# Kernel optimization log

Measured on AMD Instinct MI355X. Metric: run time of the kernel, lower is better.

## Reference

```python
import jax, jax.numpy as jnp
import numpy as np
import math

B, N, H, TDIM, K, R = 32, 4096, 256, 128, 2, 2


def setup_inputs() -> dict:
    key = jax.random.key(0)
    ks = jax.random.split(key, 12)
    s = 1.0 / math.sqrt(H)
    gain = 1.414
    return {
        "x": jax.random.normal(ks[0], (B, N), jnp.float32),
        "t": jax.random.uniform(ks[1], (B,), jnp.float32),
        # scaled so repeated L@x stays O(1) over Chebyshev hops
        "laplacian": jax.random.normal(ks[2], (N, N), jnp.float32) / math.sqrt(N),
        "w_g1": jax.random.normal(ks[3], (1, H, K + 1), jnp.float32) * gain / math.sqrt(1 + H),
        "w_g2": jax.random.normal(ks[4], (H, 1, K + 1), jnp.float32) * gain / math.sqrt(1 + H),
        "w_t1": jax.random.normal(ks[5], (TDIM, H), jnp.float32) / math.sqrt(TDIM),
        "b_t1": jnp.zeros((H,), jnp.float32),
        "w_t2": jax.random.normal(ks[6], (H, H), jnp.float32) * s,
        "b_t2": jnp.zeros((H,), jnp.float32),
        "w_map": jax.random.normal(ks[7], (N, H), jnp.float32) / math.sqrt(N),
        "b_map": jnp.zeros((H,), jnp.float32),
        "res_w": jax.random.normal(ks[8], (R, 3, H, H), jnp.float32) * s,
        "res_b": jnp.zeros((R, 3, H), jnp.float32),
        "w_o1": jax.random.normal(ks[9], (H, H), jnp.float32) * s,
        "b_o1": jnp.zeros((H,), jnp.float32),
        "w_o2": jax.random.normal(ks[10], (H, N), jnp.float32) * s,
        "b_o2": jnp.zeros((N,), jnp.float32),
    }


def timestep_embedding(t, dim, max_period=10000):
    half = dim // 2  # dim is even here
    freqs = jnp.exp(-math.log(max_period) * jnp.arange(half, dtype=t.dtype) / half)
    args = t[:, None] * freqs[None, :]  # [B, half]
    return jnp.concatenate([jnp.cos(args), jnp.sin(args)], axis=-1)  # [B, dim]


def gcn_layer(L, x, w, conv_order):
    xs = [x]
    h = x
    for _ in range(conv_order):
        h = jnp.einsum('mn,bnc->bmc', L, h)  # sparse-style Laplacian propagation (dense here)
        xs.append(h)
    X = jnp.stack(xs, axis=-1)  # [B, N, C, K+1]
    return jnp.einsum('bnik,iok->bno', X, w)


def reference(x, t, laplacian, w_g1, w_g2, w_t1, b_t1, w_t2, b_t2,
              w_map, b_map, res_w, res_b, w_o1, b_o1, w_o2, b_o2):
    silu = jax.nn.silu
    # time embedding path: sinusoidal -> Linear -> SiLU -> Linear
    temb = timestep_embedding(t, TDIM)
    t_out = silu(temb @ w_t1 + b_t1) @ w_t2 + b_t2  # [B, H]
    # GCNBlock: two Chebyshev GCN layers (GCNLayer.forward applies no activation)
    g = gcn_layer(laplacian, x[:, :, None], w_g1, K)  # [B, N, H]
    g = gcn_layer(laplacian, g, w_g2, K)[..., 0]      # [B, N]
    # ResNet_FC on the node signal
    h = g @ w_map + b_map  # [B, H]
    inv_sqrt2 = 1.0 / math.sqrt(2.0)
    for r in range(R):
        z = h
        for i in range(3):
            z = silu(z @ res_w[r, i] + res_b[r, i])
        h = (h + z) * inv_sqrt2
    # output head with time conditioning
    out = silu((h + t_out) @ w_o1 + b_o1) @ w_o2 + b_o2  # [B, N]
    return out
```

## Files before the change

### kernel.cpp

```cpp
#include <hip/hip_runtime.h>
#include <hip/hip_bf16.h>

typedef __bf16 bf16x8 __attribute__((ext_vector_type(8)));
typedef __bf16 bf16x4 __attribute__((ext_vector_type(4)));
typedef float  f32x4  __attribute__((ext_vector_type(4)));


static constexpr size_t WS_A     = 0;
static constexpr size_t WS_TOUT  = 1024;
static constexpr size_t WS_Z1    = 65536;
static constexpr size_t WS_ZSTR  = 524288;
static constexpr size_t WS_H0    = WS_Z1 + 4 * WS_ZSTR;
static constexpr size_t WS_G2F   = WS_H0 + 32768;
static constexpr size_t WS_UB    = WS_G2F + 524288;
static constexpr size_t WS_WMAPT = 2752512;
static constexpr size_t WS_WO2T  = WS_WMAPT + 2097152;
static constexpr size_t WS_LBF   = 8388608;

__device__ __forceinline__ f32x4 mfma16(bf16x8 a, bf16x8 b, f32x4 c) {
    return __builtin_amdgcn_mfma_f32_16x16x32_bf16(a, b, c, 0, 0, 0);
}

__device__ __forceinline__ bf16x8 pack8(f32x4 lo, f32x4 hi) {
    bf16x8 r;
    r[0] = (__bf16)lo[0]; r[1] = (__bf16)lo[1]; r[2] = (__bf16)lo[2]; r[3] = (__bf16)lo[3];
    r[4] = (__bf16)hi[0]; r[5] = (__bf16)hi[1]; r[6] = (__bf16)hi[2]; r[7] = (__bf16)hi[3];
    return r;
}

__device__ __forceinline__ bf16x8 cvt8(const float* p) {
    return pack8(*(const f32x4*)p, *(const f32x4*)(p + 4));
}

__device__ __forceinline__ float silu_f(float x) { return x / (1.0f + __expf(-x)); }

template <int NST>
__device__ __forceinline__ float dotW(const float* __restrict__ W,
                                      const float* __restrict__ zs, int col) {
    float wb[2][16];
#pragma unroll
    for (int u = 0; u < 16; ++u) wb[0][u] = W[u * 256 + col];
    float a0 = 0, a1 = 0, a2 = 0, a3 = 0;
#pragma unroll
    for (int g = 0; g < NST; ++g) {
        const int cur = g & 1, nxt = cur ^ 1;
        if (g < NST - 1) {
#pragma unroll
            for (int u = 0; u < 16; ++u) wb[nxt][u] = W[((g + 1) * 16 + u) * 256 + col];
        }
        const float* z = zs + g * 16;
#pragma unroll
        for (int u = 0; u < 16; u += 4) {
            a0 += z[u]     * wb[cur][u];
            a1 += z[u + 1] * wb[cur][u + 1];
            a2 += z[u + 2] * wb[cur][u + 2];
            a3 += z[u + 3] * wb[cur][u + 3];
        }
    }
    return (a0 + a1) + (a2 + a3);
}

__device__ __forceinline__ void transpose_tile(const float* __restrict__ src, int sstride,
                                               __bf16* __restrict__ dst, int dstride,
                                               int r0, int c0, float* sh, int tid) {
    const int r = tid >> 3, cg = (tid & 7) * 4;
    f32x4 v = *(const f32x4*)(src + (size_t)(r0 + r) * sstride + c0 + cg);
    sh[r * 33 + cg + 0] = v[0];
    sh[r * 33 + cg + 1] = v[1];
    sh[r * 33 + cg + 2] = v[2];
    sh[r * 33 + cg + 3] = v[3];
    __syncthreads();
    bf16x4 o;
    o[0] = (__bf16)sh[(cg + 0) * 33 + r];
    o[1] = (__bf16)sh[(cg + 1) * 33 + r];
    o[2] = (__bf16)sh[(cg + 2) * 33 + r];
    o[3] = (__bf16)sh[(cg + 3) * 33 + r];
    *(bf16x4*)(dst + (size_t)(c0 + r) * dstride + r0 + cg) = o;
}

static constexpr int PG_LCVT  = 8192;
static constexpr int PG_COEF  = PG_LCVT;
static constexpr int PG_TMLP  = PG_COEF + 1;
static constexpr int PG_WMAP  = PG_TMLP + 32;
static constexpr int PG_WO2   = PG_WMAP + 1024;
static constexpr int PG_TOTAL = PG_WO2 + 1024;

__global__ __launch_bounds__(256) void prep_kernel(
    const float* __restrict__ t, const float* __restrict__ L,
    const float* __restrict__ w_g1, const float* __restrict__ w_g2,
    const float* __restrict__ w_t1, const float* __restrict__ b_t1,
    const float* __restrict__ w_t2, const float* __restrict__ b_t2,
    const float* __restrict__ w_map, const float* __restrict__ w_o2,
    char* __restrict__ ws)
{
    __shared__ float sh[1056];
    const int bi = blockIdx.x, tid = threadIdx.x;
    if (bi < PG_LCVT) {
        const size_t base = (size_t)bi * 2048 + (size_t)tid * 8;
        *(bf16x8*)((__bf16*)(ws + WS_LBF) + base) = cvt8(L + base);
    } else if (bi == PG_COEF) {
        if (tid < 9) {
            const int k1 = tid / 3, k2 = tid % 3;
            float s = 0.f;
            for (int h = 0; h < 256; ++h) s += w_g1[h * 3 + k1] * w_g2[h * 3 + k2];
            sh[tid] = s;
        }
        __syncthreads();
        if (tid == 0) {
            float* a = (float*)(ws + WS_A);
            a[0] = sh[0];
            a[1] = sh[1] + sh[3];
            a[2] = sh[2] + sh[4] + sh[6];
            a[3] = sh[5] + sh[7];
            a[4] = sh[8];
        }
    } else if (bi < PG_WMAP) {
        const int b = bi - PG_TMLP;
        float* t_out = (float*)(ws + WS_TOUT);
        if (tid < 64) {
            float fr = __expf(-9.210340371976184f * (float)tid * (1.0f / 64.0f));
            float ang = t[b] * fr;
            sh[tid]      = __cosf(ang);
            sh[64 + tid] = __sinf(ang);
        }
        __syncthreads();
        float h1 = silu_f(b_t1[tid] + dotW<8>(w_t1, sh, tid));
        sh[128 + tid] = h1;
        __syncthreads();
        t_out[b * 256 + tid] = b_t2[tid] + dotW<16>(w_t2, sh + 128, tid);
    } else if (bi < PG_WO2) {
        const int ti = bi - PG_WMAP;
        transpose_tile(w_map, 256, (__bf16*)(ws + WS_WMAPT), 4096,
                       (ti >> 3) * 32, (ti & 7) * 32, sh, tid);
    } else {
        const int ti = bi - PG_WO2;
        transpose_tile(w_o2, 4096, (__bf16*)(ws + WS_WO2T), 256,
                       (ti & 7) * 32, (ti >> 3) * 32, sh, tid);
    }
}

__device__ __forceinline__ void hop_core(
    const __bf16* __restrict__ Lb, const float* __restrict__ zin,
    float (*red)[16][33], int bi, int tid, float v[2])
{
    const int wave = tid >> 6, lane = tid & 63;
    const int l15 = lane & 15, q = lane >> 4;
    const int m0 = bi * 16;
    const int kbase = wave * 1024 + q * 8;

    const __bf16* ap  = Lb + (size_t)(m0 + l15) * 4096 + kbase;
    const float*  b0p = zin + (size_t)l15 * 4096 + kbase;
    const float*  b1p = zin + (size_t)(l15 + 16) * 4096 + kbase;

    bf16x8 abuf[4];
    f32x4 b0lo[4], b0hi[4], b1lo[4], b1hi[4];
    f32x4 acc0 = {0,0,0,0}, acc1 = {0,0,0,0};
#pragma unroll
    for (int s = 0; s < 3; ++s) {
        const int k = s * 32;
        abuf[s] = *(const bf16x8*)(ap + k);
        b0lo[s] = *(const f32x4*)(b0p + k);
        b0hi[s] = *(const f32x4*)(b0p + k + 4);
        b1lo[s] = *(const f32x4*)(b1p + k);
        b1hi[s] = *(const f32x4*)(b1p + k + 4);
    }
#pragma unroll
    for (int s = 0; s < 32; ++s) {
        const int cur = s & 3;
        if (s < 29) {
            const int kn = (s + 3) * 32;
            const int nxt = (s + 3) & 3;
            abuf[nxt] = *(const bf16x8*)(ap + kn);
            b0lo[nxt] = *(const f32x4*)(b0p + kn);
            b0hi[nxt] = *(const f32x4*)(b0p + kn + 4);
            b1lo[nxt] = *(const f32x4*)(b1p + kn);
            b1hi[nxt] = *(const f32x4*)(b1p + kn + 4);
        }
        bf16x8 b0 = pack8(b0lo[cur], b0hi[cur]);
        bf16x8 b1 = pack8(b1lo[cur], b1hi[cur]);
        acc0 = mfma16(abuf[cur], b0, acc0);
        acc1 = mfma16(abuf[cur], b1, acc1);
    }
#pragma unroll
    for (int r = 0; r < 4; ++r) {
        const int mr = q * 4 + r;
        red[wave][mr][l15]      = acc0[r];
        red[wave][mr][l15 + 16] = acc1[r];
    }
    __syncthreads();
#pragma unroll
    for (int j = 0; j < 2; ++j) {
        const int o = tid + 256 * j;
        const int m = o & 15, bc = o >> 4;
        v[j] = red[0][m][bc] + red[1][m][bc] + red[2][m][bc] + red[3][m][bc];
    }
}

__global__ __launch_bounds__(256) void hop_kernel(
    const __bf16* __restrict__ Lb, const float* __restrict__ zin,
    float* __restrict__ zout)
{
    __shared__ float red[4][16][33];
    const int bi = blockIdx.x, tid = threadIdx.x;
    float v[2];
    hop_core(Lb, zin, red, bi, tid, v);
    const int m0 = bi * 16;
#pragma unroll
    for (int j = 0; j < 2; ++j) {
        const int o = tid + 256 * j;
        const int m = o & 15, bc = o >> 4;
        zout[(size_t)bc * 4096 + m0 + m] = v[j];
    }
}

__global__ __launch_bounds__(256) void hop_final_kernel(
    const __bf16* __restrict__ Lb, const float* __restrict__ z3,
    const float* __restrict__ x, const float* __restrict__ z1,
    const float* __restrict__ z2, const float* __restrict__ a,
    float* __restrict__ g2)
{
    __shared__ float red[4][16][33];
    const int bi = blockIdx.x, tid = threadIdx.x;
    float v[2];
    hop_core(Lb, z3, red, bi, tid, v);
    const int m0 = bi * 16;
    const float c0 = a[0], c1 = a[1], c2 = a[2], c3 = a[3], c4 = a[4];
#pragma unroll
    for (int j = 0; j < 2; ++j) {
        const int o = tid + 256 * j;
        const int m = o & 15, bc = o >> 4;
        const size_t idx = (size_t)bc * 4096 + m0 + m;
        g2[idx] = c0 * x[idx] + c1 * z1[idx] + c2 * z2[idx] + c3 * z3[idx] + c4 * v[j];
    }
}

__global__ __launch_bounds__(512) void map_gemm_kernel(
    const float* __restrict__ g2, const __bf16* __restrict__ w_mapT,
    float* __restrict__ h0)
{
    __shared__ float red[8][16][33];
    const int bi = blockIdx.x, tid = threadIdx.x;
    const int wave = tid >> 6, lane = tid & 63;
    const int l15 = lane & 15, q = lane >> 4;
    const int btile = bi & 1, hp = bi >> 1;
    const int kbase = wave * 512 + q * 8;

    const float*  ap  = g2 + (size_t)(btile * 16 + l15) * 4096 + kbase;
    const __bf16* bp0 = w_mapT + (size_t)(hp * 32 + l15) * 4096 + kbase;
    const __bf16* bp1 = w_mapT + (size_t)(hp * 32 + 16 + l15) * 4096 + kbase;

    f32x4 alo[4], ahi[4];
    bf16x8 b0b[4], b1b[4];
    f32x4 acc0 = {0,0,0,0}, acc1 = {0,0,0,0};
#pragma unroll
    for (int s = 0; s < 3; ++s) {
        const int k = s * 32;
        alo[s] = *(const f32x4*)(ap + k);
        ahi[s] = *(const f32x4*)(ap + k + 4);
        b0b[s] = *(const bf16x8*)(bp0 + k);
        b1b[s] = *(const bf16x8*)(bp1 + k);
    }
#pragma unroll
    for (int s = 0; s < 16; ++s) {
        const int cur = s & 3;
        if (s < 13) {
            const int kn = (s + 3) * 32;
            const int nxt = (s + 3) & 3;
            alo[nxt] = *(const f32x4*)(ap + kn);
            ahi[nxt] = *(const f32x4*)(ap + kn + 4);
            b0b[nxt] = *(const bf16x8*)(bp0 + kn);
            b1b[nxt] = *(const bf16x8*)(bp1 + kn);
        }
        bf16x8 av = pack8(alo[cur], ahi[cur]);
        acc0 = mfma16(av, b0b[cur], acc0);
        acc1 = mfma16(av, b1b[cur], acc1);
    }
#pragma unroll
    for (int r = 0; r < 4; ++r) {
        const int mr = q * 4 + r;
        red[wave][mr][l15]      = acc0[r];
        red[wave][mr][l15 + 16] = acc1[r];
    }
    __syncthreads();
    const int m = tid >> 5, hcol = tid & 31;
    float v = 0.f;
#pragma unroll
    for (int w = 0; w < 8; ++w) v += red[w][m][hcol];
    h0[(size_t)(btile * 16 + m) * 256 + hp * 32 + hcol] = v;
}

__global__ __launch_bounds__(1024) void resnet_kernel(
    const float* __restrict__ h0, const float* __restrict__ b_map,
    const float* __restrict__ res_w, const float* __restrict__ res_b,
    const float* __restrict__ t_out, const float* __restrict__ w_o1,
    const float* __restrict__ b_o1, __bf16* __restrict__ u_b)
{
    __shared__ float zs[256];
    __shared__ float part[4][256];
    const int b = blockIdx.x, tid = threadIdx.x;
    const int col = tid & 255, kg = tid >> 8;

    float hv = 0.f;
    if (kg == 0) {
        hv = h0[b * 256 + col] + b_map[col];
        zs[col] = hv;
    }
    __syncthreads();

#pragma unroll
    for (int r = 0; r < 2; ++r) {
        for (int i = 0; i < 3; ++i) {
            part[kg][col] = dotW<4>(res_w + ((size_t)(r * 3 + i) << 16) + (size_t)kg * 64 * 256,
                                    zs + kg * 64, col);
            __syncthreads();
            if (kg == 0) {
                zs[col] = silu_f(res_b[(r * 3 + i) * 256 + col]
                                 + part[0][col] + part[1][col] + part[2][col] + part[3][col]);
            }
            __syncthreads();
        }
        if (kg == 0) {
            hv = (hv + zs[col]) * 0.70710678118654752f;
            zs[col] = hv;
        }
        __syncthreads();
    }

    if (kg == 0) zs[col] = hv + t_out[b * 256 + col];
    __syncthreads();
    part[kg][col] = dotW<4>(w_o1 + (size_t)kg * 64 * 256, zs + kg * 64, col);
    __syncthreads();
    if (kg == 0) {
        u_b[b * 256 + col] = (__bf16)silu_f(b_o1[col]
            + part[0][col] + part[1][col] + part[2][col] + part[3][col]);
    }
}

__global__ __launch_bounds__(256) void out_gemm_kernel(
    const __bf16* __restrict__ u_b, const __bf16* __restrict__ w_o2T,
    const float* __restrict__ b_o2, float* __restrict__ out)
{
    const int tid = threadIdx.x;
    const int wave = tid >> 6, lane = tid & 63;
    const int l15 = lane & 15, q = lane >> 4;
    const int g = blockIdx.x * 4 + wave;
    const int btile = g & 1;
    const int n0 = (g >> 1) * 32;

    const __bf16* ap  = u_b + (size_t)(btile * 16 + l15) * 256;
    const __bf16* bp0 = w_o2T + (size_t)(n0 + l15) * 256;
    const __bf16* bp1 = w_o2T + (size_t)(n0 + 16 + l15) * 256;

    f32x4 acc0 = {0,0,0,0}, acc1 = {0,0,0,0};
#pragma unroll
    for (int ks = 0; ks < 8; ++ks) {
        const int k = ks * 32 + q * 8;
        bf16x8 a  = *(const bf16x8*)(ap + k);
        bf16x8 b0 = *(const bf16x8*)(bp0 + k);
        bf16x8 b1 = *(const bf16x8*)(bp1 + k);
        acc0 = mfma16(a, b0, acc0);
        acc1 = mfma16(a, b1, acc1);
    }
    const int row = btile * 16 + q * 4;
    const int na = n0 + l15, nb = n0 + 16 + l15;
#pragma unroll
    for (int r = 0; r < 4; ++r) {
        out[(size_t)(row + r) * 4096 + na] = acc0[r] + b_o2[na];
        out[(size_t)(row + r) * 4096 + nb] = acc1[r] + b_o2[nb];
    }
}

extern "C" void kernel_launch(void* const* d_in, const int* in_sizes, int n_in,
                              void* d_out, int out_size, void* d_ws, size_t ws_size,
                              hipStream_t stream)
{
    (void)in_sizes; (void)n_in; (void)out_size; (void)ws_size;
    const float* x     = (const float*)d_in[0];
    const float* t     = (const float*)d_in[1];
    const float* L     = (const float*)d_in[2];
    const float* w_g1  = (const float*)d_in[3];
    const float* w_g2  = (const float*)d_in[4];
    const float* w_t1  = (const float*)d_in[5];
    const float* b_t1  = (const float*)d_in[6];
    const float* w_t2  = (const float*)d_in[7];
    const float* b_t2  = (const float*)d_in[8];
    const float* w_map = (const float*)d_in[9];
    const float* b_map = (const float*)d_in[10];
    const float* res_w = (const float*)d_in[11];
    const float* res_b = (const float*)d_in[12];
    const float* w_o1  = (const float*)d_in[13];
    const float* b_o1  = (const float*)d_in[14];
    const float* w_o2  = (const float*)d_in[15];
    const float* b_o2  = (const float*)d_in[16];
    float* out = (float*)d_out;
    char* ws = (char*)d_ws;

    float* a_c  = (float*)(ws + WS_A);
    float* tout = (float*)(ws + WS_TOUT);
    float* z1   = (float*)(ws + WS_Z1);
    float* z2   = (float*)(ws + WS_Z1 + WS_ZSTR);
    float* z3   = (float*)(ws + WS_Z1 + 2 * WS_ZSTR);
    float* h0   = (float*)(ws + WS_H0);
    float* g2   = (float*)(ws + WS_G2F);
    __bf16* u_b    = (__bf16*)(ws + WS_UB);
    __bf16* w_mapT = (__bf16*)(ws + WS_WMAPT);
    __bf16* w_o2T  = (__bf16*)(ws + WS_WO2T);
    __bf16* Lb     = (__bf16*)(ws + WS_LBF);

    prep_kernel<<<PG_TOTAL, 256, 0, stream>>>(t, L, w_g1, w_g2, w_t1, b_t1, w_t2, b_t2,
                                              w_map, w_o2, ws);
    hop_kernel<<<256, 256, 0, stream>>>(Lb, x,  z1);
    hop_kernel<<<256, 256, 0, stream>>>(Lb, z1, z2);
    hop_kernel<<<256, 256, 0, stream>>>(Lb, z2, z3);
    hop_final_kernel<<<256, 256, 0, stream>>>(Lb, z3, x, z1, z2, a_c, g2);
    map_gemm_kernel<<<16, 512, 0, stream>>>(g2, w_mapT, h0);
    resnet_kernel<<<32, 1024, 0, stream>>>(h0, b_map, res_w, res_b, tout, w_o1, b_o1, u_b);
    out_gemm_kernel<<<64, 256, 0, stream>>>(u_b, w_o2T, b_o2, out);
}
```

Measured before the change: 283.4 us.

## Fuse Laplacian bf16 conversion into first hop and keep hop intermediates in bf16

```diff
diff --git a/kernel.cpp b/kernel.cpp
--- a/kernel.cpp
+++ b/kernel.cpp
@@ -8,12 +8,12 @@
 
 static constexpr size_t WS_A     = 0;
 static constexpr size_t WS_TOUT  = 1024;
-static constexpr size_t WS_Z1    = 65536;
-static constexpr size_t WS_ZSTR  = 524288;
-static constexpr size_t WS_H0    = WS_Z1 + 4 * WS_ZSTR;
-static constexpr size_t WS_G2F   = WS_H0 + 32768;
-static constexpr size_t WS_UB    = WS_G2F + 524288;
-static constexpr size_t WS_WMAPT = 2752512;
+static constexpr size_t WS_ZB    = 65536;
+static constexpr size_t WS_ZSTR  = 262144;
+static constexpr size_t WS_G2B   = WS_ZB + 3 * WS_ZSTR;
+static constexpr size_t WS_H0    = WS_G2B + 262144;
+static constexpr size_t WS_UB    = WS_H0 + 32768;
+static constexpr size_t WS_WMAPT = 1179648;
 static constexpr size_t WS_WO2T  = WS_WMAPT + 2097152;
 static constexpr size_t WS_LBF   = 8388608;
 
@@ -26,10 +26,6 @@
     r[0] = (__bf16)lo[0]; r[1] = (__bf16)lo[1]; r[2] = (__bf16)lo[2]; r[3] = (__bf16)lo[3];
     r[4] = (__bf16)hi[0]; r[5] = (__bf16)hi[1]; r[6] = (__bf16)hi[2]; r[7] = (__bf16)hi[3];
     return r;
-}
-
-__device__ __forceinline__ bf16x8 cvt8(const float* p) {
-    return pack8(*(const f32x4*)p, *(const f32x4*)(p + 4));
 }
 
 __device__ __forceinline__ float silu_f(float x) { return x / (1.0f + __expf(-x)); }
@@ -78,15 +74,8 @@
     *(bf16x4*)(dst + (size_t)(c0 + r) * dstride + r0 + cg) = o;
 }
 
-static constexpr int PG_LCVT  = 8192;
-static constexpr int PG_COEF  = PG_LCVT;
-static constexpr int PG_TMLP  = PG_COEF + 1;
-static constexpr int PG_WMAP  = PG_TMLP + 32;
-static constexpr int PG_WO2   = PG_WMAP + 1024;
-static constexpr int PG_TOTAL = PG_WO2 + 1024;
-
 __global__ __launch_bounds__(256) void prep_kernel(
-    const float* __restrict__ t, const float* __restrict__ L,
+    const float* __restrict__ t,
     const float* __restrict__ w_g1, const float* __restrict__ w_g2,
     const float* __restrict__ w_t1, const float* __restrict__ b_t1,
     const float* __restrict__ w_t2, const float* __restrict__ b_t2,
@@ -95,10 +84,7 @@
 {
     __shared__ float sh[1056];
     const int bi = blockIdx.x, tid = threadIdx.x;
-    if (bi < PG_LCVT) {
-        const size_t base = (size_t)bi * 2048 + (size_t)tid * 8;
-        *(bf16x8*)((__bf16*)(ws + WS_LBF) + base) = cvt8(L + base);
-    } else if (bi == PG_COEF) {
+    if (bi == 0) {
         if (tid < 9) {
             const int k1 = tid / 3, k2 = tid % 3;
             float s = 0.f;
@@ -114,8 +100,8 @@
             a[3] = sh[5] + sh[7];
             a[4] = sh[8];
         }
-    } else if (bi < PG_WMAP) {
-        const int b = bi - PG_TMLP;
+    } else if (bi < 33) {
+        const int b = bi - 1;
         float* t_out = (float*)(ws + WS_TOUT);
         if (tid < 64) {
             float fr = __expf(-9.210340371976184f * (float)tid * (1.0f / 64.0f));
@@ -128,58 +114,58 @@
         sh[128 + tid] = h1;
         __syncthreads();
         t_out[b * 256 + tid] = b_t2[tid] + dotW<16>(w_t2, sh + 128, tid);
-    } else if (bi < PG_WO2) {
-        const int ti = bi - PG_WMAP;
+    } else if (bi < 1057) {
+        const int ti = bi - 33;
         transpose_tile(w_map, 256, (__bf16*)(ws + WS_WMAPT), 4096,
                        (ti >> 3) * 32, (ti & 7) * 32, sh, tid);
     } else {
-        const int ti = bi - PG_WO2;
+        const int ti = bi - 1057;
         transpose_tile(w_o2, 4096, (__bf16*)(ws + WS_WO2T), 256,
                        (ti & 7) * 32, (ti >> 3) * 32, sh, tid);
     }
 }
 
-__device__ __forceinline__ void hop_core(
-    const __bf16* __restrict__ Lb, const float* __restrict__ zin,
-    float (*red)[16][33], int bi, int tid, float v[2])
-{
+__global__ __launch_bounds__(512) void hop1_kernel(
+    const float* __restrict__ L, const float* __restrict__ x,
+    __bf16* __restrict__ Lb, __bf16* __restrict__ z1b)
+{
+    __shared__ float red[8][16][33];
+    const int bi = blockIdx.x, tid = threadIdx.x;
     const int wave = tid >> 6, lane = tid & 63;
     const int l15 = lane & 15, q = lane >> 4;
     const int m0 = bi * 16;
-    const int kbase = wave * 1024 + q * 8;
-
-    const __bf16* ap  = Lb + (size_t)(m0 + l15) * 4096 + kbase;
-    const float*  b0p = zin + (size_t)l15 * 4096 + kbase;
-    const float*  b1p = zin + (size_t)(l15 + 16) * 4096 + kbase;
-
-    bf16x8 abuf[4];
-    f32x4 b0lo[4], b0hi[4], b1lo[4], b1hi[4];
+    const int kbase = wave * 512 + q * 8;
+
+    const float* ap  = L + (size_t)(m0 + l15) * 4096 + kbase;
+    __bf16*      lbp = Lb + (size_t)(m0 + l15) * 4096 + kbase;
+    const float* b0p = x + (size_t)l15 * 4096 + kbase;
+    const float* b1p = x + (size_t)(l15 + 16) * 4096 + kbase;
+
+    f32x4 alo[3], ahi[3], b0lo[3], b0hi[3], b1lo[3], b1hi[3];
     f32x4 acc0 = {0,0,0,0}, acc1 = {0,0,0,0};
 #pragma unroll
-    for (int s = 0; s < 3; ++s) {
+    for (int s = 0; s < 2; ++s) {
         const int k = s * 32;
-        abuf[s] = *(const bf16x8*)(ap + k);
-        b0lo[s] = *(const f32x4*)(b0p + k);
-        b0hi[s] = *(const f32x4*)(b0p + k + 4);
-        b1lo[s] = *(const f32x4*)(b1p + k);
-        b1hi[s] = *(const f32x4*)(b1p + k + 4);
-    }
-#pragma unroll
-    for (int s = 0; s < 32; ++s) {
-        const int cur = s & 3;
-        if (s < 29) {
-            const int kn = (s + 3) * 32;
-            const int nxt = (s + 3) & 3;
-            abuf[nxt] = *(const bf16x8*)(ap + kn);
-            b0lo[nxt] = *(const f32x4*)(b0p + kn);
-            b0hi[nxt] = *(const f32x4*)(b0p + kn + 4);
-            b1lo[nxt] = *(const f32x4*)(b1p + kn);
-            b1hi[nxt] = *(const f32x4*)(b1p + kn + 4);
-        }
+        alo[s]  = *(const f32x4*)(ap + k);   ahi[s]  = *(const f32x4*)(ap + k + 4);
+        b0lo[s] = *(const f32x4*)(b0p + k);  b0hi[s] = *(const f32x4*)(b0p + k + 4);
+        b1lo[s] = *(const f32x4*)(b1p + k);  b1hi[s] = *(const f32x4*)(b1p + k + 4);
+    }
+#pragma unroll
+    for (int s = 0; s < 16; ++s) {
+        const int cur = s % 3;
+        if (s < 14) {
+            const int nxt = (s + 2) % 3;
+            const int kn = (s + 2) * 32;
+            alo[nxt]  = *(const f32x4*)(ap + kn);   ahi[nxt]  = *(const f32x4*)(ap + kn + 4);
+            b0lo[nxt] = *(const f32x4*)(b0p + kn);  b0hi[nxt] = *(const f32x4*)(b0p + kn + 4);
+            b1lo[nxt] = *(const f32x4*)(b1p + kn);  b1hi[nxt] = *(const f32x4*)(b1p + kn + 4);
+        }
+        bf16x8 av = pack8(alo[cur], ahi[cur]);
+        *(bf16x8*)(lbp + s * 32) = av;
         bf16x8 b0 = pack8(b0lo[cur], b0hi[cur]);
         bf16x8 b1 = pack8(b1lo[cur], b1hi[cur]);
-        acc0 = mfma16(abuf[cur], b0, acc0);
-        acc1 = mfma16(abuf[cur], b1, acc1);
+        acc0 = mfma16(av, b0, acc0);
+        acc1 = mfma16(av, b1, acc1);
     }
 #pragma unroll
     for (int r = 0; r < 4; ++r) {
@@ -188,54 +174,122 @@
         red[wave][mr][l15 + 16] = acc1[r];
     }
     __syncthreads();
-#pragma unroll
-    for (int j = 0; j < 2; ++j) {
-        const int o = tid + 256 * j;
-        const int m = o & 15, bc = o >> 4;
-        v[j] = red[0][m][bc] + red[1][m][bc] + red[2][m][bc] + red[3][m][bc];
-    }
-}
-
-__global__ __launch_bounds__(256) void hop_kernel(
-    const __bf16* __restrict__ Lb, const float* __restrict__ zin,
-    float* __restrict__ zout)
-{
-    __shared__ float red[4][16][33];
+    const int m = tid & 15, bc = tid >> 4;
+    float v = 0.f;
+#pragma unroll
+    for (int w = 0; w < 8; ++w) v += red[w][m][bc];
+    z1b[(size_t)bc * 4096 + m0 + m] = (__bf16)v;
+}
+
+__global__ __launch_bounds__(512) void hop_kernel(
+    const __bf16* __restrict__ Lb, const __bf16* __restrict__ zin,
+    __bf16* __restrict__ zout)
+{
+    __shared__ float red[8][16][33];
     const int bi = blockIdx.x, tid = threadIdx.x;
-    float v[2];
-    hop_core(Lb, zin, red, bi, tid, v);
+    const int wave = tid >> 6, lane = tid & 63;
+    const int l15 = lane & 15, q = lane >> 4;
     const int m0 = bi * 16;
-#pragma unroll
-    for (int j = 0; j < 2; ++j) {
-        const int o = tid + 256 * j;
-        const int m = o & 15, bc = o >> 4;
-        zout[(size_t)bc * 4096 + m0 + m] = v[j];
-    }
-}
-
-__global__ __launch_bounds__(256) void hop_final_kernel(
-    const __bf16* __restrict__ Lb, const float* __restrict__ z3,
-    const float* __restrict__ x, const float* __restrict__ z1,
-    const float* __restrict__ z2, const float* __restrict__ a,
-    float* __restrict__ g2)
-{
-    __shared__ float red[4][16][33];
+    const int kbase = wave * 512 + q * 8;
+
+    const __bf16* ap  = Lb + (size_t)(m0 + l15) * 4096 + kbase;
+    const __bf16* b0p = zin + (size_t)l15 * 4096 + kbase;
+    const __bf16* b1p = zin + (size_t)(l15 + 16) * 4096 + kbase;
+
+    bf16x8 ab[4], b0b[4], b1b[4];
+    f32x4 acc0 = {0,0,0,0}, acc1 = {0,0,0,0};
+#pragma unroll
+    for (int s = 0; s < 3; ++s) {
+        const int k = s * 32;
+        ab[s]  = *(const bf16x8*)(ap + k);
+        b0b[s] = *(const bf16x8*)(b0p + k);
+        b1b[s] = *(const bf16x8*)(b1p + k);
+    }
+#pragma unroll
+    for (int s = 0; s < 16; ++s) {
+        const int cur = s & 3;
+        if (s < 13) {
+            const int nxt = (s + 3) & 3;
+            const int kn = (s + 3) * 32;
+            ab[nxt]  = *(const bf16x8*)(ap + kn);
+            b0b[nxt] = *(const bf16x8*)(b0p + kn);
+            b1b[nxt] = *(const bf16x8*)(b1p + kn);
+        }
+        acc0 = mfma16(ab[cur], b0b[cur], acc0);
+        acc1 = mfma16(ab[cur], b1b[cur], acc1);
+    }
+#pragma unroll
+    for (int r = 0; r < 4; ++r) {
+        const int mr = q * 4 + r;
+        red[wave][mr][l15]      = acc0[r];
+        red[wave][mr][l15 + 16] = acc1[r];
+    }
+    __syncthreads();
+    const int m = tid & 15, bc = tid >> 4;
+    float v = 0.f;
+#pragma unroll
+    for (int w = 0; w < 8; ++w) v += red[w][m][bc];
+    zout[(size_t)bc * 4096 + m0 + m] = (__bf16)v;
+}
+
+__global__ __launch_bounds__(512) void hop_final_kernel(
+    const __bf16* __restrict__ Lb, const __bf16* __restrict__ z3b,
+    const float* __restrict__ x, const __bf16* __restrict__ z1b,
+    const __bf16* __restrict__ z2b, const float* __restrict__ a,
+    __bf16* __restrict__ g2b)
+{
+    __shared__ float red[8][16][33];
     const int bi = blockIdx.x, tid = threadIdx.x;
-    float v[2];
-    hop_core(Lb, z3, red, bi, tid, v);
+    const int wave = tid >> 6, lane = tid & 63;
+    const int l15 = lane & 15, q = lane >> 4;
     const int m0 = bi * 16;
+    const int kbase = wave * 512 + q * 8;
+
+    const __bf16* ap  = Lb + (size_t)(m0 + l15) * 4096 + kbase;
+    const __bf16* b0p = z3b + (size_t)l15 * 4096 + kbase;
+    const __bf16* b1p = z3b + (size_t)(l15 + 16) * 4096 + kbase;
+
+    bf16x8 ab[4], b0b[4], b1b[4];
+    f32x4 acc0 = {0,0,0,0}, acc1 = {0,0,0,0};
+#pragma unroll
+    for (int s = 0; s < 3; ++s) {
+        const int k = s * 32;
+        ab[s]  = *(const bf16x8*)(ap + k);
+        b0b[s] = *(const bf16x8*)(b0p + k);
+        b1b[s] = *(const bf16x8*)(b1p + k);
+    }
+#pragma unroll
+    for (int s = 0; s < 16; ++s) {
+        const int cur = s & 3;
+        if (s < 13) {
+            const int nxt = (s + 3) & 3;
+            const int kn = (s + 3) * 32;
+            ab[nxt]  = *(const bf16x8*)(ap + kn);
+            b0b[nxt] = *(const bf16x8*)(b0p + kn);
+            b1b[nxt] = *(const bf16x8*)(b1p + kn);
+        }
+        acc0 = mfma16(ab[cur], b0b[cur], acc0);
+        acc1 = mfma16(ab[cur], b1b[cur], acc1);
+    }
+#pragma unroll
+    for (int r = 0; r < 4; ++r) {
+        const int mr = q * 4 + r;
+        red[wave][mr][l15]      = acc0[r];
+        red[wave][mr][l15 + 16] = acc1[r];
+    }
+    __syncthreads();
+    const int m = tid & 15, bc = tid >> 4;
+    float v = 0.f;
+#pragma unroll
+    for (int w = 0; w < 8; ++w) v += red[w][m][bc];
     const float c0 = a[0], c1 = a[1], c2 = a[2], c3 = a[3], c4 = a[4];
-#pragma unroll
-    for (int j = 0; j < 2; ++j) {
-        const int o = tid + 256 * j;
-        const int m = o & 15, bc = o >> 4;
-        const size_t idx = (size_t)bc * 4096 + m0 + m;
-        g2[idx] = c0 * x[idx] + c1 * z1[idx] + c2 * z2[idx] + c3 * z3[idx] + c4 * v[j];
-    }
+    const size_t idx = (size_t)bc * 4096 + m0 + m;
+    g2b[idx] = (__bf16)(c0 * x[idx] + c1 * (float)z1b[idx] + c2 * (float)z2b[idx]
+                        + c3 * (float)z3b[idx] + c4 * v);
 }
 
 __global__ __launch_bounds__(512) void map_gemm_kernel(
-    const float* __restrict__ g2, const __bf16* __restrict__ w_mapT,
+    const __bf16* __restrict__ g2b, const __bf16* __restrict__ w_mapT,
     float* __restrict__ h0)
 {
     __shared__ float red[8][16][33];
@@ -245,18 +299,16 @@
     const int btile = bi & 1, hp = bi >> 1;
     const int kbase = wave * 512 + q * 8;
 
-    const float*  ap  = g2 + (size_t)(btile * 16 + l15) * 4096 + kbase;
+    const __bf16* ap  = g2b + (size_t)(btile * 16 + l15) * 4096 + kbase;
     const __bf16* bp0 = w_mapT + (size_t)(hp * 32 + l15) * 4096 + kbase;
     const __bf16* bp1 = w_mapT + (size_t)(hp * 32 + 16 + l15) * 4096 + kbase;
 
-    f32x4 alo[4], ahi[4];
-    bf16x8 b0b[4], b1b[4];
+    bf16x8 ab[4], b0b[4], b1b[4];
     f32x4 acc0 = {0,0,0,0}, acc1 = {0,0,0,0};
 #pragma unroll
     for (int s = 0; s < 3; ++s) {
         const int k = s * 32;
-        alo[s] = *(const f32x4*)(ap + k);
-        ahi[s] = *(const f32x4*)(ap + k + 4);
+        ab[s]  = *(const bf16x8*)(ap + k);
         b0b[s] = *(const bf16x8*)(bp0 + k);
         b1b[s] = *(const bf16x8*)(bp1 + k);
     }
@@ -264,16 +316,14 @@
     for (int s = 0; s < 16; ++s) {
         const int cur = s & 3;
         if (s < 13) {
+            const int nxt = (s + 3) & 3;
             const int kn = (s + 3) * 32;
-            const int nxt = (s + 3) & 3;
-            alo[nxt] = *(const f32x4*)(ap + kn);
-            ahi[nxt] = *(const f32x4*)(ap + kn + 4);
+            ab[nxt]  = *(const bf16x8*)(ap + kn);
             b0b[nxt] = *(const bf16x8*)(bp0 + kn);
             b1b[nxt] = *(const bf16x8*)(bp1 + kn);
         }
-        bf16x8 av = pack8(alo[cur], ahi[cur]);
-        acc0 = mfma16(av, b0b[cur], acc0);
-        acc1 = mfma16(av, b1b[cur], acc1);
+        acc0 = mfma16(ab[cur], b0b[cur], acc0);
+        acc1 = mfma16(ab[cur], b1b[cur], acc1);
     }
 #pragma unroll
     for (int r = 0; r < 4; ++r) {
@@ -397,23 +447,23 @@
 
     float* a_c  = (float*)(ws + WS_A);
     float* tout = (float*)(ws + WS_TOUT);
-    float* z1   = (float*)(ws + WS_Z1);
-    float* z2   = (float*)(ws + WS_Z1 + WS_ZSTR);
-    float* z3   = (float*)(ws + WS_Z1 + 2 * WS_ZSTR);
+    __bf16* z1b = (__bf16*)(ws + WS_ZB);
+    __bf16* z2b = (__bf16*)(ws + WS_ZB + WS_ZSTR);
+    __bf16* z3b = (__bf16*)(ws + WS_ZB + 2 * WS_ZSTR);
+    __bf16* g2b = (__bf16*)(ws + WS_G2B);
     float* h0   = (float*)(ws + WS_H0);
-    float* g2   = (float*)(ws + WS_G2F);
     __bf16* u_b    = (__bf16*)(ws + WS_UB);
     __bf16* w_mapT = (__bf16*)(ws + WS_WMAPT);
     __bf16* w_o2T  = (__bf16*)(ws + WS_WO2T);
     __bf16* Lb     = (__bf16*)(ws + WS_LBF);
 
-    prep_kernel<<<PG_TOTAL, 256, 0, stream>>>(t, L, w_g1, w_g2, w_t1, b_t1, w_t2, b_t2,
-                                              w_map, w_o2, ws);
-    hop_kernel<<<256, 256, 0, stream>>>(Lb, x,  z1);
-    hop_kernel<<<256, 256, 0, stream>>>(Lb, z1, z2);
-    hop_kernel<<<256, 256, 0, stream>>>(Lb, z2, z3);
-    hop_final_kernel<<<256, 256, 0, stream>>>(Lb, z3, x, z1, z2, a_c, g2);
-    map_gemm_kernel<<<16, 512, 0, stream>>>(g2, w_mapT, h0);
+    prep_kernel<<<2081, 256, 0, stream>>>(t, w_g1, w_g2, w_t1, b_t1, w_t2, b_t2,
+                                          w_map, w_o2, ws);
+    hop1_kernel<<<256, 512, 0, stream>>>(L, x, Lb, z1b);
+    hop_kernel<<<256, 512, 0, stream>>>(Lb, z1b, z2b);
+    hop_kernel<<<256, 512, 0, stream>>>(Lb, z2b, z3b);
+    hop_final_kernel<<<256, 512, 0, stream>>>(Lb, z3b, x, z1b, z2b, a_c, g2b);
+    map_gemm_kernel<<<16, 512, 0, stream>>>(g2b, w_mapT, h0);
     resnet_kernel<<<32, 1024, 0, stream>>>(h0, b_map, res_w, res_b, tout, w_o1, b_o1, u_b);
     out_gemm_kernel<<<64, 256, 0, stream>>>(u_b, w_o2T, b_o2, out);
 }
```

Result: faster. 253.0 us (-10.7%).
